# Optimization experiments

Hardware: AMD Instinct MI355X
Metric: run time of the kernel (lower is better)

The kernel has to match this reference:

```python
import jax, jax.numpy as jnp
import numpy as np

B, NI, LS, D, H, W, LAB = 512, 256, 64, 8, 128, 256, 10
L = LS - 1          # logsig_dim - 1 (leading term dropped)
NSTEPS = 256        # fixed Tsit5 steps over [t0, t1]

# Tsit5 Butcher tableau (Tsitouras 2011)
C2, C3, C4, C5, C6 = 0.161, 0.327, 0.9, 0.9800255409045097, 1.0
A21 = 0.161
A31, A32 = -0.008480655492356989, 0.335480655492357
A41, A42, A43 = 2.8971530571054935, -6.359448489975075, 4.3622954328695815
A51, A52, A53, A54 = 5.325864828439257, -11.748883564062828, 7.4955393428898365, -0.09249506636175525
A61, A62, A63, A64, A65 = 5.86145544294642, -12.92096931784711, 8.159367898576159, -0.071584973281401, -0.028269050394068383
B1, B2, B3, B4, B5, B6 = 0.09646076681806523, 0.01, 0.4798896504144996, 1.379008574103742, -3.290069515436081, 2.324710524099774


def setup_inputs() -> dict:
    key = jax.random.key(0)
    ks = jax.random.split(key, 8)

    def lin(k, out_d, in_d):  # eqx.nn.Linear default init: U(-1/sqrt(in), 1/sqrt(in))
        kw, kb = jax.random.split(k)
        lim = 1.0 / np.sqrt(in_d)
        Wm = jax.random.uniform(kw, (out_d, in_d), minval=-lim, maxval=lim, dtype=jnp.float32)
        bv = jax.random.uniform(kb, (out_d,), minval=-lim, maxval=lim, dtype=jnp.float32)
        return Wm, bv

    W0, b0 = lin(ks[0], W, H)        # VF MLP layer 1
    W1, b1 = lin(ks[1], W, W)        # VF MLP layer 2
    W2, b2 = lin(ks[2], H * L, W)    # VF MLP output layer
    l1w, l1b = lin(ks[3], H, D)      # linear1
    l2w, l2b = lin(ks[4], LAB, H)    # linear2

    ts = jnp.linspace(0.0, 1.0, NI + 1, dtype=jnp.float32)
    intervals = ts[1:]               # right endpoints for searchsorted lookup
    logsig = 0.1 * jax.random.normal(ks[5], (B, NI, LS), dtype=jnp.float32)
    x0 = jax.random.normal(ks[6], (B, D), dtype=jnp.float32)
    return dict(ts=ts, intervals=intervals, logsig=logsig, x0=x0,
                W0=W0, b0=b0, W1=W1, b1=b1, W2=W2, b2=b2,
                l1w=l1w, l1b=l1b, l2w=l2w, l2b=l2b)


def _forward(ts, intervals, logsig, x0, W0, b0, W1, b1, W2, b2, l1w, l1b, l2w, l2b):
    def f(t, y):  # y: [B, H] -> dy/dt: [B, H]
        idx = jnp.clip(jnp.searchsorted(intervals, t), 0, NI - 1)
        h = jax.nn.silu(y @ W0.T + b0)
        h = jax.nn.silu(h @ W1.T + b1)
        A = jnp.tanh(h @ W2.T + b2).reshape(-1, H, L)   # [B, H, L]
        g = logsig[:, idx, 1:]                           # [B, L]
        return jnp.einsum('bhl,bl->bh', A, g)

    y0 = x0 @ l1w.T + l1b                                # linear1
    dt = (ts[-1] - ts[0]) / NSTEPS

    @jax.checkpoint
    def step(carry, _):
        t, y = carry
        k1 = f(t, y)
        k2 = f(t + C2 * dt, y + dt * (A21 * k1))
        k3 = f(t + C3 * dt, y + dt * (A31 * k1 + A32 * k2))
        k4 = f(t + C4 * dt, y + dt * (A41 * k1 + A42 * k2 + A43 * k3))
        k5 = f(t + C5 * dt, y + dt * (A51 * k1 + A52 * k2 + A53 * k3 + A54 * k4))
        k6 = f(t + C6 * dt, y + dt * (A61 * k1 + A62 * k2 + A63 * k3 + A64 * k4 + A65 * k5))
        y_new = y + dt * (B1 * k1 + B2 * k2 + B3 * k3 + B4 * k4 + B5 * k5 + B6 * k6)
        return (t + dt, y_new), None

    (_, yf), _ = jax.lax.scan(step, (ts[0], y0), None, length=NSTEPS)
    return jax.nn.softmax(yf @ l2w.T + l2b, axis=-1)     # classification head


def reference(ts, intervals, logsig, x0, W0, b0, W1, b1, W2, b2, l1w, l1b, l2w, l2b):
    return _forward(ts, intervals, logsig, x0, W0, b0, W1, b1, W2, b2, l1w, l1b, l2w, l2b)
```

## Files before the change

### kernel.cpp

```cpp
#include <hip/hip_runtime.h>

typedef __attribute__((ext_vector_type(8))) short short8;
typedef __attribute__((ext_vector_type(4))) float f32x4;

#define DT (1.0f/256.0f)
#define NSTEPS 256

__device__ __forceinline__ short f2bf(float f) {
    unsigned u = __float_as_uint(f);
    u = (u + 0x7fffu + ((u >> 16) & 1u)) >> 16;
    return (short)u;
}

__device__ __forceinline__ float fast_tanh(float x) {
    float e = __expf(2.f * x);
    return 1.f - __fdividef(2.f, e + 1.f);
}

__global__ void perm_w0(const float* __restrict__ W0, short* __restrict__ W0p) {
    int i = blockIdx.x * 256 + threadIdx.x;
    int j = i & 7, l = (i >> 3) & 63, kc = (i >> 9) & 3, ot = i >> 11;
    int row = ot * 16 + (l & 15);
    int col = kc * 32 + ((l >> 4) << 3) + j;
    W0p[i] = f2bf(W0[row * 128 + col]);
}
__global__ void perm_w1(const float* __restrict__ W1, short* __restrict__ W1p) {
    int i = blockIdx.x * 256 + threadIdx.x;
    int j = i & 7, l = (i >> 3) & 63, kc = (i >> 9) & 7, ot = i >> 12;
    int row = ot * 16 + (l & 15);
    int col = kc * 32 + ((l >> 4) << 3) + j;
    W1p[i] = f2bf(W1[row * 256 + col]);
}
__global__ void perm_w2(const float* __restrict__ W2, short* __restrict__ W2p) {
    int i = blockIdx.x * 256 + threadIdx.x;
    int j = i & 7, ln = (i >> 3) & 63, kc = (i >> 9) & 7;
    int v = i >> 12;
    int ht = v >> 6, lv = v & 63;
    if (lv == 63) { W2p[i] = 0; return; }
    int row = (ht * 16 + (ln & 15)) * 63 + lv;
    int col = kc * 32 + ((ln >> 4) << 3) + j;
    W2p[i] = f2bf(W2[row * 256 + col]);
}

__global__ void y0_kernel(const float* __restrict__ x0, const float* __restrict__ l1w,
                          const float* __restrict__ l1b, float* __restrict__ y) {
    int i = blockIdx.x * 256 + threadIdx.x;
    int b = i >> 7, h = i & 127;
    float s = l1b[h];
    #pragma unroll
    for (int d = 0; d < 8; ++d) s += x0[b * 8 + d] * l1w[h * 8 + d];
    y[i] = s;
}

template<int STAGE>
__global__ __launch_bounds__(512, 2) void stage_kernel(
    const float* __restrict__ ycur, float* __restrict__ ynext,
    float* __restrict__ kbuf,
    const short* __restrict__ W0p, const short* __restrict__ W1p, const short* __restrict__ W2p,
    const float* __restrict__ b0, const float* __restrict__ b1, const float* __restrict__ b2,
    const float* __restrict__ logsig, int idx)
{
    __shared__ __align__(16) short ysb[16 * 136];
    __shared__ __align__(16) short h1b[16 * 264];
    __shared__ __align__(16) short h2b[16 * 264];
    __shared__ float gsh[16 * 65];
    __shared__ float b2sh[16 * 65];
    __shared__ float b0sh[256];
    __shared__ float b1sh[256];
    __shared__ float kred[8][16][17];

    const int tid  = threadIdx.x;
    const int bg   = blockIdx.x >> 3;
    const int ht   = blockIdx.x & 7;
    const int w    = tid >> 6;
    const int lane = tid & 63;
    const int q    = lane >> 4;
    const int rr   = lane & 15;

    if (tid < 256) {
        const int r  = tid >> 4;
        const int c8 = (tid & 15) * 8;
        const float4* yp = reinterpret_cast<const float4*>(ycur + (bg * 16 + r) * 128 + c8);
        float4 a = yp[0], bq = yp[1];
        float v[8] = {a.x, a.y, a.z, a.w, bq.x, bq.y, bq.z, bq.w};
        if constexpr (STAGE >= 2) {
            constexpr float cf[5][5] = {
                {0.161f, 0.f, 0.f, 0.f, 0.f},
                {-0.008480655492356989f, 0.335480655492357f, 0.f, 0.f, 0.f},
                {2.8971530571054935f, -6.359448489975075f, 4.3622954328695815f, 0.f, 0.f},
                {5.325864828439257f, -11.748883564062828f, 7.4955393428898365f, -0.09249506636175525f, 0.f},
                {5.86145544294642f, -12.92096931784711f, 8.159367898576159f, -0.071584973281401f, -0.028269050394068383f}};
            #pragma unroll
            for (int kk = 0; kk < STAGE - 1; ++kk) {
                const float4* kp = reinterpret_cast<const float4*>(kbuf + kk * 65536 + (bg * 16 + r) * 128 + c8);
                float4 ka = kp[0], kb2 = kp[1];
                float kv[8] = {ka.x, ka.y, ka.z, ka.w, kb2.x, kb2.y, kb2.z, kb2.w};
                float c = DT * cf[STAGE - 2][kk];
                #pragma unroll
                for (int ii = 0; ii < 8; ++ii) v[ii] += c * kv[ii];
            }
        }
        short8 sv;
        #pragma unroll
        for (int ii = 0; ii < 8; ++ii) sv[ii] = f2bf(v[ii]);
        *reinterpret_cast<short8*>(&ysb[r * 136 + c8]) = sv;
    } else {
        const int t2 = tid - 256;
        b0sh[t2] = b0[t2];
        b1sh[t2] = b1[t2];
        int r2 = t2 >> 4, seg = t2 & 15, l0 = seg * 4;
        if (l0 < 63) {
            int n = (l0 + 4 <= 63) ? 4 : (63 - l0);
            const float* gp = logsig + (bg * 16 + r2) * 16384 + idx * 64 + 1 + l0;
            const float* bp = b2 + (ht * 16 + r2) * 63 + l0;
            for (int ii = 0; ii < n; ++ii) {
                gsh[r2 * 65 + l0 + ii]  = gp[ii];
                b2sh[r2 * 65 + l0 + ii] = bp[ii];
            }
            if (seg == 15) {
                gsh[r2 * 65 + 63]  = 0.f;
                b2sh[r2 * 65 + 63] = 0.f;
            }
        }
    }
    __syncthreads();

    #pragma unroll
    for (int oi = 0; oi < 2; ++oi) {
        int ot = w * 2 + oi;
        f32x4 acc0 = {0.f, 0.f, 0.f, 0.f}, acc1 = {0.f, 0.f, 0.f, 0.f};
        #pragma unroll
        for (int kc = 0; kc < 2; ++kc) {
            short8 af0 = *reinterpret_cast<const short8*>(W0p + (ot * 4 + kc) * 512 + lane * 8);
            short8 bf0 = *reinterpret_cast<const short8*>(&ysb[rr * 136 + kc * 32 + q * 8]);
            acc0 = __builtin_amdgcn_mfma_f32_16x16x32_bf16(af0, bf0, acc0, 0, 0, 0);
            short8 af1 = *reinterpret_cast<const short8*>(W0p + (ot * 4 + kc + 2) * 512 + lane * 8);
            short8 bf1 = *reinterpret_cast<const short8*>(&ysb[rr * 136 + (kc + 2) * 32 + q * 8]);
            acc1 = __builtin_amdgcn_mfma_f32_16x16x32_bf16(af1, bf1, acc1, 0, 0, 0);
        }
        int ob = ot * 16 + q * 4;
        float vv[4];
        #pragma unroll
        for (int jj = 0; jj < 4; ++jj) {
            float x = acc0[jj] + acc1[jj] + b0sh[ob + jj];
            vv[jj] = x * __fdividef(1.f, 1.f + __expf(-x));
        }
        unsigned lo = (unsigned)(unsigned short)f2bf(vv[0]) | ((unsigned)(unsigned short)f2bf(vv[1]) << 16);
        unsigned hi = (unsigned)(unsigned short)f2bf(vv[2]) | ((unsigned)(unsigned short)f2bf(vv[3]) << 16);
        *reinterpret_cast<unsigned*>(&h1b[rr * 264 + ob])     = lo;
        *reinterpret_cast<unsigned*>(&h1b[rr * 264 + ob + 2]) = hi;
    }
    __syncthreads();

    #pragma unroll
    for (int oi = 0; oi < 2; ++oi) {
        int ot = w * 2 + oi;
        f32x4 acc0 = {0.f, 0.f, 0.f, 0.f}, acc1 = {0.f, 0.f, 0.f, 0.f};
        #pragma unroll
        for (int kc = 0; kc < 4; ++kc) {
            short8 af0 = *reinterpret_cast<const short8*>(W1p + (ot * 8 + kc) * 512 + lane * 8);
            short8 bf0 = *reinterpret_cast<const short8*>(&h1b[rr * 264 + kc * 32 + q * 8]);
            acc0 = __builtin_amdgcn_mfma_f32_16x16x32_bf16(af0, bf0, acc0, 0, 0, 0);
            short8 af1 = *reinterpret_cast<const short8*>(W1p + (ot * 8 + kc + 4) * 512 + lane * 8);
            short8 bf1 = *reinterpret_cast<const short8*>(&h1b[rr * 264 + (kc + 4) * 32 + q * 8]);
            acc1 = __builtin_amdgcn_mfma_f32_16x16x32_bf16(af1, bf1, acc1, 0, 0, 0);
        }
        int ob = ot * 16 + q * 4;
        float vv[4];
        #pragma unroll
        for (int jj = 0; jj < 4; ++jj) {
            float x = acc0[jj] + acc1[jj] + b1sh[ob + jj];
            vv[jj] = x * __fdividef(1.f, 1.f + __expf(-x));
        }
        unsigned lo = (unsigned)(unsigned short)f2bf(vv[0]) | ((unsigned)(unsigned short)f2bf(vv[1]) << 16);
        unsigned hi = (unsigned)(unsigned short)f2bf(vv[2]) | ((unsigned)(unsigned short)f2bf(vv[3]) << 16);
        *reinterpret_cast<unsigned*>(&h2b[rr * 264 + ob])     = lo;
        *reinterpret_cast<unsigned*>(&h2b[rr * 264 + ob + 2]) = hi;
    }
    __syncthreads();

    float kacc[4] = {0.f, 0.f, 0.f, 0.f};
    const int lvbase = w * 8;
    #pragma unroll
    for (int i2 = 0; i2 < 4; ++i2) {
        const int lvA = lvbase + i2 * 2;
        const int lvB = lvA + 1;
        f32x4 aA0 = {0.f,0.f,0.f,0.f}, aA1 = {0.f,0.f,0.f,0.f};
        f32x4 aB0 = {0.f,0.f,0.f,0.f}, aB1 = {0.f,0.f,0.f,0.f};
        const short* wpA = W2p + (size_t)((ht * 64 + lvA) * 8) * 512 + lane * 8;
        const short* wpB = wpA + 8 * 512;
        #pragma unroll
        for (int kc = 0; kc < 4; ++kc) {
            short8 bf0 = *reinterpret_cast<const short8*>(&h2b[rr * 264 + kc * 32 + q * 8]);
            short8 bf1 = *reinterpret_cast<const short8*>(&h2b[rr * 264 + (kc + 4) * 32 + q * 8]);
            aA0 = __builtin_amdgcn_mfma_f32_16x16x32_bf16(*reinterpret_cast<const short8*>(wpA + kc * 512),       bf0, aA0, 0, 0, 0);
            aA1 = __builtin_amdgcn_mfma_f32_16x16x32_bf16(*reinterpret_cast<const short8*>(wpA + (kc + 4) * 512), bf1, aA1, 0, 0, 0);
            aB0 = __builtin_amdgcn_mfma_f32_16x16x32_bf16(*reinterpret_cast<const short8*>(wpB + kc * 512),       bf0, aB0, 0, 0, 0);
            aB1 = __builtin_amdgcn_mfma_f32_16x16x32_bf16(*reinterpret_cast<const short8*>(wpB + (kc + 4) * 512), bf1, aB1, 0, 0, 0);
        }
        float gA = gsh[rr * 65 + lvA];
        float gB = gsh[rr * 65 + lvB];
        #pragma unroll
        for (int jj = 0; jj < 4; ++jj) {
            float xA = aA0[jj] + aA1[jj] + b2sh[(q * 4 + jj) * 65 + lvA];
            kacc[jj] += fast_tanh(xA) * gA;
            float xB = aB0[jj] + aB1[jj] + b2sh[(q * 4 + jj) * 65 + lvB];
            kacc[jj] += fast_tanh(xB) * gB;
        }
    }
    #pragma unroll
    for (int jj = 0; jj < 4; ++jj) kred[w][q * 4 + jj][rr] = kacc[jj];
    __syncthreads();

    if (tid < 256) {
        int bl = tid >> 4;
        int hl = tid & 15;
        float s = kred[0][hl][bl] + kred[1][hl][bl] + kred[2][hl][bl] + kred[3][hl][bl]
                + kred[4][hl][bl] + kred[5][hl][bl] + kred[6][hl][bl] + kred[7][hl][bl];
        int gi = (bg * 16 + bl) * 128 + ht * 16 + hl;
        if constexpr (STAGE < 6) {
            kbuf[(STAGE - 1) * 65536 + gi] = s;
        } else {
            float k1v = kbuf[0 * 65536 + gi], k2v = kbuf[1 * 65536 + gi], k3v = kbuf[2 * 65536 + gi],
                  k4v = kbuf[3 * 65536 + gi], k5v = kbuf[4 * 65536 + gi];
            ynext[gi] = ycur[gi] + DT * (0.09646076681806523f * k1v + 0.01f * k2v
                        + 0.4798896504144996f * k3v + 1.379008574103742f * k4v
                        + (-3.290069515436081f) * k5v + 2.324710524099774f * s);
        }
    }
}

__global__ void out_kernel(const float* __restrict__ yf, const float* __restrict__ l2w,
                           const float* __restrict__ l2b, float* __restrict__ out) {
    int b = blockIdx.x, t = threadIdx.x;
    float ya = yf[b * 128 + t], yb = yf[b * 128 + 64 + t];
    __shared__ float lg[10];
    for (int c = 0; c < 10; ++c) {
        float p = ya * l2w[c * 128 + t] + yb * l2w[c * 128 + 64 + t];
        for (int off = 32; off > 0; off >>= 1) p += __shfl_down(p, off);
        if (t == 0) lg[c] = p + l2b[c];
    }
    __syncthreads();
    if (t == 0) {
        float m = lg[0];
        for (int c = 1; c < 10; ++c) m = fmaxf(m, lg[c]);
        float s = 0.f, e[10];
        for (int c = 0; c < 10; ++c) { e[c] = expf(lg[c] - m); s += e[c]; }
        for (int c = 0; c < 10; ++c) out[b * 10 + c] = e[c] / s;
    }
}

extern "C" void kernel_launch(void* const* d_in, const int* in_sizes, int n_in,
                              void* d_out, int out_size, void* d_ws, size_t ws_size,
                              hipStream_t stream) {
    const float* logsig = (const float*)d_in[2];
    const float* x0  = (const float*)d_in[3];
    const float* W0  = (const float*)d_in[4];
    const float* b0  = (const float*)d_in[5];
    const float* W1  = (const float*)d_in[6];
    const float* b1  = (const float*)d_in[7];
    const float* W2  = (const float*)d_in[8];
    const float* b2  = (const float*)d_in[9];
    const float* l1w = (const float*)d_in[10];
    const float* l1b = (const float*)d_in[11];
    const float* l2w = (const float*)d_in[12];
    const float* l2b = (const float*)d_in[13];
    float* out = (float*)d_out;

    char* ws = (char*)d_ws;
    float* yb0  = (float*)(ws);
    float* yb1  = (float*)(ws + 262144);
    float* kbuf = (float*)(ws + 524288);
    short* W0p  = (short*)(ws + 2097152);
    short* W1p  = (short*)(ws + 2162688);
    short* W2p  = (short*)(ws + 2424832);

    perm_w0<<<128, 256, 0, stream>>>(W0, W0p);
    perm_w1<<<512, 256, 0, stream>>>(W1, W1p);
    perm_w2<<<8192, 256, 0, stream>>>(W2, W2p);
    y0_kernel<<<256, 256, 0, stream>>>(x0, l1w, l1b, yb0);

    for (int s = 0; s < NSTEPS; ++s) {
        float* yc = (s & 1) ? yb1 : yb0;
        float* yn = (s & 1) ? yb0 : yb1;
        int i1 = (s == 0) ? 0 : (s - 1);
        stage_kernel<1><<<256, 512, 0, stream>>>(yc, nullptr, kbuf, W0p, W1p, W2p, b0, b1, b2, logsig, i1);
        stage_kernel<2><<<256, 512, 0, stream>>>(yc, nullptr, kbuf, W0p, W1p, W2p, b0, b1, b2, logsig, s);
        stage_kernel<3><<<256, 512, 0, stream>>>(yc, nullptr, kbuf, W0p, W1p, W2p, b0, b1, b2, logsig, s);
        stage_kernel<4><<<256, 512, 0, stream>>>(yc, nullptr, kbuf, W0p, W1p, W2p, b0, b1, b2, logsig, s);
        stage_kernel<5><<<256, 512, 0, stream>>>(yc, nullptr, kbuf, W0p, W1p, W2p, b0, b1, b2, logsig, s);
        stage_kernel<6><<<256, 512, 0, stream>>>(yc, yn,      kbuf, W0p, W1p, W2p, b0, b1, b2, logsig, s);
    }
    out_kernel<<<512, 64, 0, stream>>>(yb0, l2w, l2b, out);
}
```

Baseline: 16.29 ms.

## Replace per-stage kernel launches with a persistent cooperative kernel using group barriers

```diff
diff --git a/kernel.cpp b/kernel.cpp
--- a/kernel.cpp
+++ b/kernel.cpp
@@ -1,6 +1,7 @@
 #include <hip/hip_runtime.h>
 
 typedef __attribute__((ext_vector_type(8))) short short8;
+typedef __attribute__((ext_vector_type(4))) short short4e;
 typedef __attribute__((ext_vector_type(4))) float f32x4;
 
 #define DT (1.0f/256.0f)
@@ -15,6 +16,13 @@
 __device__ __forceinline__ float fast_tanh(float x) {
     float e = __expf(2.f * x);
     return 1.f - __fdividef(2.f, e + 1.f);
+}
+
+__device__ __forceinline__ float ld_agent(const float* p) {
+    return __hip_atomic_load(p, __ATOMIC_RELAXED, __HIP_MEMORY_SCOPE_AGENT);
+}
+__device__ __forceinline__ void st_agent(float* p, float v) {
+    __hip_atomic_store(p, v, __ATOMIC_RELAXED, __HIP_MEMORY_SCOPE_AGENT);
 }
 
 __global__ void perm_w0(const float* __restrict__ W0, short* __restrict__ W0p) {
@@ -52,37 +60,38 @@
     y[i] = s;
 }
 
+struct Smem {
+    alignas(16) short ysb[16 * 136];
+    alignas(16) short h1b[16 * 264];
+    alignas(16) short h2b[16 * 264];
+    float gsh[16 * 65];
+    float b2sh[16 * 65];
+    float b0sh[256];
+    float b1sh[256];
+    float kred[8][16][17];
+};
+
 template<int STAGE>
-__global__ __launch_bounds__(512, 2) void stage_kernel(
+__device__ __forceinline__ void do_stage(
+    Smem& sm, int s, int bg, int ht, int tid,
     const float* __restrict__ ycur, float* __restrict__ ynext,
     float* __restrict__ kbuf,
     const short* __restrict__ W0p, const short* __restrict__ W1p, const short* __restrict__ W2p,
-    const float* __restrict__ b0, const float* __restrict__ b1, const float* __restrict__ b2,
-    const float* __restrict__ logsig, int idx)
+    const float* __restrict__ logsig,
+    unsigned* __restrict__ barctr, int phase)
 {
-    __shared__ __align__(16) short ysb[16 * 136];
-    __shared__ __align__(16) short h1b[16 * 264];
-    __shared__ __align__(16) short h2b[16 * 264];
-    __shared__ float gsh[16 * 65];
-    __shared__ float b2sh[16 * 65];
-    __shared__ float b0sh[256];
-    __shared__ float b1sh[256];
-    __shared__ float kred[8][16][17];
-
-    const int tid  = threadIdx.x;
-    const int bg   = blockIdx.x >> 3;
-    const int ht   = blockIdx.x & 7;
     const int w    = tid >> 6;
     const int lane = tid & 63;
     const int q    = lane >> 4;
     const int rr   = lane & 15;
 
-    if (tid < 256) {
-        const int r  = tid >> 4;
-        const int c8 = (tid & 15) * 8;
-        const float4* yp = reinterpret_cast<const float4*>(ycur + (bg * 16 + r) * 128 + c8);
-        float4 a = yp[0], bq = yp[1];
-        float v[8] = {a.x, a.y, a.z, a.w, bq.x, bq.y, bq.z, bq.w};
+    {
+        const int r  = tid >> 5;
+        const int c4 = (tid & 31) * 4;
+        const float* yrow = ycur + (bg * 16 + r) * 128 + c4;
+        float v[4];
+        #pragma unroll
+        for (int ii = 0; ii < 4; ++ii) v[ii] = ld_agent(yrow + ii);
         if constexpr (STAGE >= 2) {
             constexpr float cf[5][5] = {
                 {0.161f, 0.f, 0.f, 0.f, 0.f},
@@ -92,35 +101,22 @@
                 {5.86145544294642f, -12.92096931784711f, 8.159367898576159f, -0.071584973281401f, -0.028269050394068383f}};
             #pragma unroll
             for (int kk = 0; kk < STAGE - 1; ++kk) {
-                const float4* kp = reinterpret_cast<const float4*>(kbuf + kk * 65536 + (bg * 16 + r) * 128 + c8);
-                float4 ka = kp[0], kb2 = kp[1];
-                float kv[8] = {ka.x, ka.y, ka.z, ka.w, kb2.x, kb2.y, kb2.z, kb2.w};
-                float c = DT * cf[STAGE - 2][kk];
+                const float c = DT * cf[STAGE - 2][kk];
+                const float* kr = kbuf + kk * 65536 + (bg * 16 + r) * 128 + c4;
                 #pragma unroll
-                for (int ii = 0; ii < 8; ++ii) v[ii] += c * kv[ii];
+                for (int ii = 0; ii < 4; ++ii) v[ii] += c * ld_agent(kr + ii);
             }
         }
-        short8 sv;
-        #pragma unroll
-        for (int ii = 0; ii < 8; ++ii) sv[ii] = f2bf(v[ii]);
-        *reinterpret_cast<short8*>(&ysb[r * 136 + c8]) = sv;
-    } else {
-        const int t2 = tid - 256;
-        b0sh[t2] = b0[t2];
-        b1sh[t2] = b1[t2];
-        int r2 = t2 >> 4, seg = t2 & 15, l0 = seg * 4;
-        if (l0 < 63) {
-            int n = (l0 + 4 <= 63) ? 4 : (63 - l0);
-            const float* gp = logsig + (bg * 16 + r2) * 16384 + idx * 64 + 1 + l0;
-            const float* bp = b2 + (ht * 16 + r2) * 63 + l0;
-            for (int ii = 0; ii < n; ++ii) {
-                gsh[r2 * 65 + l0 + ii]  = gp[ii];
-                b2sh[r2 * 65 + l0 + ii] = bp[ii];
-            }
-            if (seg == 15) {
-                gsh[r2 * 65 + 63]  = 0.f;
-                b2sh[r2 * 65 + 63] = 0.f;
-            }
+        short4e sv;
+        #pragma unroll
+        for (int ii = 0; ii < 4; ++ii) sv[ii] = f2bf(v[ii]);
+        *reinterpret_cast<short4e*>(&sm.ysb[r * 136 + c4]) = sv;
+
+        if constexpr (STAGE == 2) {
+            const int l0 = (tid & 31) * 2;
+            const float* gp = logsig + (bg * 16 + r) * 16384 + s * 64 + 1;
+            sm.gsh[r * 65 + l0]     = (l0 < 63)     ? gp[l0]     : 0.f;
+            sm.gsh[r * 65 + l0 + 1] = (l0 + 1 < 63) ? gp[l0 + 1] : 0.f;
         }
     }
     __syncthreads();
@@ -132,23 +128,23 @@
         #pragma unroll
         for (int kc = 0; kc < 2; ++kc) {
             short8 af0 = *reinterpret_cast<const short8*>(W0p + (ot * 4 + kc) * 512 + lane * 8);
-            short8 bf0 = *reinterpret_cast<const short8*>(&ysb[rr * 136 + kc * 32 + q * 8]);
+            short8 bf0 = *reinterpret_cast<const short8*>(&sm.ysb[rr * 136 + kc * 32 + q * 8]);
             acc0 = __builtin_amdgcn_mfma_f32_16x16x32_bf16(af0, bf0, acc0, 0, 0, 0);
             short8 af1 = *reinterpret_cast<const short8*>(W0p + (ot * 4 + kc + 2) * 512 + lane * 8);
-            short8 bf1 = *reinterpret_cast<const short8*>(&ysb[rr * 136 + (kc + 2) * 32 + q * 8]);
+            short8 bf1 = *reinterpret_cast<const short8*>(&sm.ysb[rr * 136 + (kc + 2) * 32 + q * 8]);
             acc1 = __builtin_amdgcn_mfma_f32_16x16x32_bf16(af1, bf1, acc1, 0, 0, 0);
         }
         int ob = ot * 16 + q * 4;
         float vv[4];
         #pragma unroll
         for (int jj = 0; jj < 4; ++jj) {
-            float x = acc0[jj] + acc1[jj] + b0sh[ob + jj];
+            float x = acc0[jj] + acc1[jj] + sm.b0sh[ob + jj];
             vv[jj] = x * __fdividef(1.f, 1.f + __expf(-x));
         }
         unsigned lo = (unsigned)(unsigned short)f2bf(vv[0]) | ((unsigned)(unsigned short)f2bf(vv[1]) << 16);
         unsigned hi = (unsigned)(unsigned short)f2bf(vv[2]) | ((unsigned)(unsigned short)f2bf(vv[3]) << 16);
-        *reinterpret_cast<unsigned*>(&h1b[rr * 264 + ob])     = lo;
-        *reinterpret_cast<unsigned*>(&h1b[rr * 264 + ob + 2]) = hi;
+        *reinterpret_cast<unsigned*>(&sm.h1b[rr * 264 + ob])     = lo;
+        *reinterpret_cast<unsigned*>(&sm.h1b[rr * 264 + ob + 2]) = hi;
     }
     __syncthreads();
 
@@ -159,23 +155,23 @@
         #pragma unroll
         for (int kc = 0; kc < 4; ++kc) {
             short8 af0 = *reinterpret_cast<const short8*>(W1p + (ot * 8 + kc) * 512 + lane * 8);
-            short8 bf0 = *reinterpret_cast<const short8*>(&h1b[rr * 264 + kc * 32 + q * 8]);
+            short8 bf0 = *reinterpret_cast<const short8*>(&sm.h1b[rr * 264 + kc * 32 + q * 8]);
             acc0 = __builtin_amdgcn_mfma_f32_16x16x32_bf16(af0, bf0, acc0, 0, 0, 0);
             short8 af1 = *reinterpret_cast<const short8*>(W1p + (ot * 8 + kc + 4) * 512 + lane * 8);
-            short8 bf1 = *reinterpret_cast<const short8*>(&h1b[rr * 264 + (kc + 4) * 32 + q * 8]);
+            short8 bf1 = *reinterpret_cast<const short8*>(&sm.h1b[rr * 264 + (kc + 4) * 32 + q * 8]);
             acc1 = __builtin_amdgcn_mfma_f32_16x16x32_bf16(af1, bf1, acc1, 0, 0, 0);
         }
         int ob = ot * 16 + q * 4;
         float vv[4];
         #pragma unroll
         for (int jj = 0; jj < 4; ++jj) {
-            float x = acc0[jj] + acc1[jj] + b1sh[ob + jj];
+            float x = acc0[jj] + acc1[jj] + sm.b1sh[ob + jj];
             vv[jj] = x * __fdividef(1.f, 1.f + __expf(-x));
         }
         unsigned lo = (unsigned)(unsigned short)f2bf(vv[0]) | ((unsigned)(unsigned short)f2bf(vv[1]) << 16);
         unsigned hi = (unsigned)(unsigned short)f2bf(vv[2]) | ((unsigned)(unsigned short)f2bf(vv[3]) << 16);
-        *reinterpret_cast<unsigned*>(&h2b[rr * 264 + ob])     = lo;
-        *reinterpret_cast<unsigned*>(&h2b[rr * 264 + ob + 2]) = hi;
+        *reinterpret_cast<unsigned*>(&sm.h2b[rr * 264 + ob])     = lo;
+        *reinterpret_cast<unsigned*>(&sm.h2b[rr * 264 + ob + 2]) = hi;
     }
     __syncthreads();
 
@@ -191,42 +187,90 @@
         const short* wpB = wpA + 8 * 512;
         #pragma unroll
         for (int kc = 0; kc < 4; ++kc) {
-            short8 bf0 = *reinterpret_cast<const short8*>(&h2b[rr * 264 + kc * 32 + q * 8]);
-            short8 bf1 = *reinterpret_cast<const short8*>(&h2b[rr * 264 + (kc + 4) * 32 + q * 8]);
+            short8 bf0 = *reinterpret_cast<const short8*>(&sm.h2b[rr * 264 + kc * 32 + q * 8]);
+            short8 bf1 = *reinterpret_cast<const short8*>(&sm.h2b[rr * 264 + (kc + 4) * 32 + q * 8]);
             aA0 = __builtin_amdgcn_mfma_f32_16x16x32_bf16(*reinterpret_cast<const short8*>(wpA + kc * 512),       bf0, aA0, 0, 0, 0);
             aA1 = __builtin_amdgcn_mfma_f32_16x16x32_bf16(*reinterpret_cast<const short8*>(wpA + (kc + 4) * 512), bf1, aA1, 0, 0, 0);
             aB0 = __builtin_amdgcn_mfma_f32_16x16x32_bf16(*reinterpret_cast<const short8*>(wpB + kc * 512),       bf0, aB0, 0, 0, 0);
             aB1 = __builtin_amdgcn_mfma_f32_16x16x32_bf16(*reinterpret_cast<const short8*>(wpB + (kc + 4) * 512), bf1, aB1, 0, 0, 0);
         }
-        float gA = gsh[rr * 65 + lvA];
-        float gB = gsh[rr * 65 + lvB];
+        float gA = sm.gsh[rr * 65 + lvA];
+        float gB = sm.gsh[rr * 65 + lvB];
         #pragma unroll
         for (int jj = 0; jj < 4; ++jj) {
-            float xA = aA0[jj] + aA1[jj] + b2sh[(q * 4 + jj) * 65 + lvA];
+            float xA = aA0[jj] + aA1[jj] + sm.b2sh[(q * 4 + jj) * 65 + lvA];
             kacc[jj] += fast_tanh(xA) * gA;
-            float xB = aB0[jj] + aB1[jj] + b2sh[(q * 4 + jj) * 65 + lvB];
+            float xB = aB0[jj] + aB1[jj] + sm.b2sh[(q * 4 + jj) * 65 + lvB];
             kacc[jj] += fast_tanh(xB) * gB;
         }
     }
     #pragma unroll
-    for (int jj = 0; jj < 4; ++jj) kred[w][q * 4 + jj][rr] = kacc[jj];
+    for (int jj = 0; jj < 4; ++jj) sm.kred[w][q * 4 + jj][rr] = kacc[jj];
     __syncthreads();
 
     if (tid < 256) {
         int bl = tid >> 4;
         int hl = tid & 15;
-        float s = kred[0][hl][bl] + kred[1][hl][bl] + kred[2][hl][bl] + kred[3][hl][bl]
-                + kred[4][hl][bl] + kred[5][hl][bl] + kred[6][hl][bl] + kred[7][hl][bl];
+        float ssum = sm.kred[0][hl][bl] + sm.kred[1][hl][bl] + sm.kred[2][hl][bl] + sm.kred[3][hl][bl]
+                   + sm.kred[4][hl][bl] + sm.kred[5][hl][bl] + sm.kred[6][hl][bl] + sm.kred[7][hl][bl];
         int gi = (bg * 16 + bl) * 128 + ht * 16 + hl;
         if constexpr (STAGE < 6) {
-            kbuf[(STAGE - 1) * 65536 + gi] = s;
+            st_agent(&kbuf[(STAGE - 1) * 65536 + gi], ssum);
         } else {
-            float k1v = kbuf[0 * 65536 + gi], k2v = kbuf[1 * 65536 + gi], k3v = kbuf[2 * 65536 + gi],
-                  k4v = kbuf[3 * 65536 + gi], k5v = kbuf[4 * 65536 + gi];
-            ynext[gi] = ycur[gi] + DT * (0.09646076681806523f * k1v + 0.01f * k2v
+            float k1v = ld_agent(&kbuf[0 * 65536 + gi]), k2v = ld_agent(&kbuf[1 * 65536 + gi]),
+                  k3v = ld_agent(&kbuf[2 * 65536 + gi]), k4v = ld_agent(&kbuf[3 * 65536 + gi]),
+                  k5v = ld_agent(&kbuf[4 * 65536 + gi]);
+            float yv = ld_agent(&ycur[gi]);
+            st_agent(&ynext[gi], yv + DT * (0.09646076681806523f * k1v + 0.01f * k2v
                         + 0.4798896504144996f * k3v + 1.379008574103742f * k4v
-                        + (-3.290069515436081f) * k5v + 2.324710524099774f * s);
-        }
+                        + (-3.290069515436081f) * k5v + 2.324710524099774f * ssum));
+        }
+    }
+
+    __syncthreads();
+    if (tid == 0) {
+        __hip_atomic_fetch_add(&barctr[bg * 16], 1u, __ATOMIC_RELEASE, __HIP_MEMORY_SCOPE_AGENT);
+        const unsigned target = 8u * (unsigned)phase;
+        while (__hip_atomic_load(&barctr[bg * 16], __ATOMIC_ACQUIRE, __HIP_MEMORY_SCOPE_AGENT) < target) { }
+    }
+    __syncthreads();
+}
+
+__global__ __launch_bounds__(512, 2) void rde_persistent(
+    float* yb0, float* yb1, float* kbuf, unsigned* barctr,
+    const short* W0p, const short* W1p, const short* W2p,
+    const float* b0, const float* b1, const float* b2,
+    const float* logsig)
+{
+    __shared__ Smem sm;
+    const int tid = threadIdx.x;
+    const int bg  = blockIdx.x >> 3;
+    const int ht  = blockIdx.x & 7;
+
+    if (tid < 256) sm.b0sh[tid] = b0[tid];
+    else           sm.b1sh[tid - 256] = b1[tid - 256];
+    {
+        const int r  = tid >> 5;
+        const int l0 = (tid & 31) * 2;
+        const float* bp = b2 + (ht * 16 + r) * 63;
+        sm.b2sh[r * 65 + l0]     = (l0 < 63)     ? bp[l0]     : 0.f;
+        sm.b2sh[r * 65 + l0 + 1] = (l0 + 1 < 63) ? bp[l0 + 1] : 0.f;
+        const float* gp = logsig + (bg * 16 + r) * 16384 + 0 * 64 + 1;
+        sm.gsh[r * 65 + l0]      = (l0 < 63)     ? gp[l0]     : 0.f;
+        sm.gsh[r * 65 + l0 + 1]  = (l0 + 1 < 63) ? gp[l0 + 1] : 0.f;
+    }
+
+    int phase = 1;
+    #pragma unroll 1
+    for (int s = 0; s < NSTEPS; ++s) {
+        const float* yc = (s & 1) ? yb1 : yb0;
+        float*       yn = (s & 1) ? yb0 : yb1;
+        do_stage<1>(sm, s, bg, ht, tid, yc, nullptr, kbuf, W0p, W1p, W2p, logsig, barctr, phase); ++phase;
+        do_stage<2>(sm, s, bg, ht, tid, yc, nullptr, kbuf, W0p, W1p, W2p, logsig, barctr, phase); ++phase;
+        do_stage<3>(sm, s, bg, ht, tid, yc, nullptr, kbuf, W0p, W1p, W2p, logsig, barctr, phase); ++phase;
+        do_stage<4>(sm, s, bg, ht, tid, yc, nullptr, kbuf, W0p, W1p, W2p, logsig, barctr, phase); ++phase;
+        do_stage<5>(sm, s, bg, ht, tid, yc, nullptr, kbuf, W0p, W1p, W2p, logsig, barctr, phase); ++phase;
+        do_stage<6>(sm, s, bg, ht, tid, yc, yn,      kbuf, W0p, W1p, W2p, logsig, barctr, phase); ++phase;
     }
 }
 
@@ -268,28 +312,22 @@
     float* out = (float*)d_out;
 
     char* ws = (char*)d_ws;
-    float* yb0  = (float*)(ws);
-    float* yb1  = (float*)(ws + 262144);
-    float* kbuf = (float*)(ws + 524288);
-    short* W0p  = (short*)(ws + 2097152);
-    short* W1p  = (short*)(ws + 2162688);
-    short* W2p  = (short*)(ws + 2424832);
-
+    float*    yb0    = (float*)(ws);
+    float*    yb1    = (float*)(ws + 262144);
+    float*    kbuf   = (float*)(ws + 524288);
+    short*    W0p    = (short*)(ws + 2097152);
+    short*    W1p    = (short*)(ws + 2162688);
+    short*    W2p    = (short*)(ws + 2424832);
+    unsigned* barctr = (unsigned*)(ws + 6619136);
+
+    hipMemsetAsync(barctr, 0, 32 * 16 * sizeof(unsigned), stream);
     perm_w0<<<128, 256, 0, stream>>>(W0, W0p);
     perm_w1<<<512, 256, 0, stream>>>(W1, W1p);
     perm_w2<<<8192, 256, 0, stream>>>(W2, W2p);
     y0_kernel<<<256, 256, 0, stream>>>(x0, l1w, l1b, yb0);
 
-    for (int s = 0; s < NSTEPS; ++s) {
-        float* yc = (s & 1) ? yb1 : yb0;
-        float* yn = (s & 1) ? yb0 : yb1;
-        int i1 = (s == 0) ? 0 : (s - 1);
-        stage_kernel<1><<<256, 512, 0, stream>>>(yc, nullptr, kbuf, W0p, W1p, W2p, b0, b1, b2, logsig, i1);
-        stage_kernel<2><<<256, 512, 0, stream>>>(yc, nullptr, kbuf, W0p, W1p, W2p, b0, b1, b2, logsig, s);
-        stage_kernel<3><<<256, 512, 0, stream>>>(yc, nullptr, kbuf, W0p, W1p, W2p, b0, b1, b2, logsig, s);
-        stage_kernel<4><<<256, 512, 0, stream>>>(yc, nullptr, kbuf, W0p, W1p, W2p, b0, b1, b2, logsig, s);
-        stage_kernel<5><<<256, 512, 0, stream>>>(yc, nullptr, kbuf, W0p, W1p, W2p, b0, b1, b2, logsig, s);
-        stage_kernel<6><<<256, 512, 0, stream>>>(yc, yn,      kbuf, W0p, W1p, W2p, b0, b1, b2, logsig, s);
-    }
+    void* args[] = {&yb0, &yb1, &kbuf, &barctr, &W0p, &W1p, &W2p, &b0, &b1, &b2, &logsig};
+    hipLaunchCooperativeKernel((const void*)rde_persistent, dim3(256), dim3(512), args, 0, stream);
+
     out_kernel<<<512, 64, 0, stream>>>(yb0, l2w, l2b, out);
 }
```

After: 30.73 ms. 88.7% more time.
